# Kernel optimization log

Measured on AMD Instinct MI355X. Metric: run time of the kernel, lower is better.

The kernel has to match this reference:

```python
import jax, jax.numpy as jnp
import numpy as np

B, L, D, H = 2, 1024, 1024, 16
HD = D // H
HIDDEN = 4 * D
EPS = 1e-6
SCALE = HD ** -0.5

# RoPE tables (head_dim is even, so rope_dim == head_dim)
_inv_freq = 1.0 / (10000.0 ** (np.arange(0, HD, 2, dtype=np.float32) / HD))
_freqs = np.arange(L, dtype=np.float32)[:, None] * _inv_freq[None, :]          # [L, HD/2]
COS = jnp.asarray(np.concatenate([np.cos(_freqs), np.cos(_freqs)], -1))        # [L, HD]
SIN = jnp.asarray(np.concatenate([np.sin(_freqs), np.sin(_freqs)], -1))
MASK = jnp.tril(jnp.ones((L, L), dtype=bool))                                   # causal


def _clin(xr, xi, Wr, Wi, br=None, bi=None):
    # complex linear: (a+bi)(c+di), weights stored [out, in] as in torch
    r = xr @ Wr.T - xi @ Wi.T
    i = xr @ Wi.T + xi @ Wr.T
    if br is not None:
        r = r + br
        i = i + bi
    return r, i


def _cln(xr, xi, gr, gi, br, bi):
    mr = xr.mean(-1, keepdims=True)
    mi = xi.mean(-1, keepdims=True)
    cr = xr - mr
    ci = xi - mi
    var = (cr * cr + ci * ci).mean(-1, keepdims=True)
    s = jnp.sqrt(var + EPS)
    nr = cr / s
    ni = ci / s
    return nr * gr - ni * gi + br, nr * gi + ni * gr + bi


def _rot_half(x):
    h = x.shape[-1] // 2
    return jnp.concatenate([-x[..., h:], x[..., :h]], -1)


def _rope(xr, xi):
    # apply same real rotation to real and imag parts (matches torch code)
    return (xr * COS + _rot_half(xr) * SIN, xi * COS + _rot_half(xi) * SIN)


def _split_heads(x):
    return x.reshape(B, L, H, HD).transpose(0, 2, 1, 3)  # [B,H,L,HD]


def _merge_heads(x):
    return x.transpose(0, 2, 1, 3).reshape(B, L, D)


def setup_inputs() -> dict:
    key = jax.random.key(0)
    ks = jax.random.split(key, 20)
    n = lambda k, shape, s=1.0: jax.random.normal(k, shape, dtype=jnp.float32) * s
    s_attn = (2.0 * (D + D)) ** -0.5
    s_fc1 = (2.0 * (D + HIDDEN)) ** -0.5
    s_fc2 = (2.0 * (HIDDEN + D)) ** -0.5
    return {
        'x_real': n(ks[0], (B, L, D)),
        'x_imag': n(ks[1], (B, L, D)),
        'Wq_r': n(ks[2], (D, D), s_attn), 'Wq_i': n(ks[3], (D, D), s_attn),
        'Wk_r': n(ks[4], (D, D), s_attn), 'Wk_i': n(ks[5], (D, D), s_attn),
        'Wv_r': n(ks[6], (D, D), s_attn), 'Wv_i': n(ks[7], (D, D), s_attn),
        'Wo_r': n(ks[8], (D, D), s_attn), 'Wo_i': n(ks[9], (D, D), s_attn),
        'bo_r': jnp.zeros((D,), jnp.float32), 'bo_i': jnp.zeros((D,), jnp.float32),
        'ln1_gr': jnp.ones((D,), jnp.float32), 'ln1_gi': jnp.zeros((D,), jnp.float32),
        'ln1_br': jnp.zeros((D,), jnp.float32), 'ln1_bi': jnp.zeros((D,), jnp.float32),
        'ln2_gr': jnp.ones((D,), jnp.float32), 'ln2_gi': jnp.zeros((D,), jnp.float32),
        'ln2_br': jnp.zeros((D,), jnp.float32), 'ln2_bi': jnp.zeros((D,), jnp.float32),
        'W1_r': n(ks[10], (HIDDEN, D), s_fc1), 'W1_i': n(ks[11], (HIDDEN, D), s_fc1),
        'b1_r': jnp.zeros((HIDDEN,), jnp.float32), 'b1_i': jnp.zeros((HIDDEN,), jnp.float32),
        'W2_r': n(ks[12], (D, HIDDEN), s_fc2), 'W2_i': n(ks[13], (D, HIDDEN), s_fc2),
        'b2_r': jnp.zeros((D,), jnp.float32), 'b2_i': jnp.zeros((D,), jnp.float32),
        'mod_b': n(ks[14], (HIDDEN,), 0.1),
    }


def reference(x_real, x_imag,
              Wq_r, Wq_i, Wk_r, Wk_i, Wv_r, Wv_i, Wo_r, Wo_i, bo_r, bo_i,
              ln1_gr, ln1_gi, ln1_br, ln1_bi, ln2_gr, ln2_gi, ln2_br, ln2_bi,
              W1_r, W1_i, b1_r, b1_i, W2_r, W2_i, b2_r, b2_i, mod_b):
    # --- attention sublayer (pre-LN) ---
    hr, hi = _cln(x_real, x_imag, ln1_gr, ln1_gi, ln1_br, ln1_bi)
    Qr, Qi = _clin(hr, hi, Wq_r, Wq_i)
    Kr, Ki = _clin(hr, hi, Wk_r, Wk_i)
    Vr, Vi = _clin(hr, hi, Wv_r, Wv_i)
    Qr, Qi, Kr, Ki = map(_split_heads, (Qr, Qi, Kr, Ki))
    Vr, Vi = _split_heads(Vr), _split_heads(Vi)
    Qr, Qi = _rope(Qr, Qi)
    Kr, Ki = _rope(Kr, Ki)
    # Hermitian inner product real part: Re(Q K*) = Qr.Kr + Qi.Ki
    scores = (jnp.einsum('bhld,bhmd->bhlm', Qr, Kr)
              + jnp.einsum('bhld,bhmd->bhlm', Qi, Ki)) * SCALE
    scores = jnp.where(MASK, scores, -jnp.inf)
    attn = jax.nn.softmax(scores, axis=-1)
    out_r = _merge_heads(jnp.einsum('bhlm,bhmd->bhld', attn, Vr))
    out_i = _merge_heads(jnp.einsum('bhlm,bhmd->bhld', attn, Vi))
    out_r, out_i = _clin(out_r, out_i, Wo_r, Wo_i, bo_r, bo_i)
    ar = x_real + out_r
    ai = x_imag + out_i
    # --- feed-forward sublayer (pre-LN) ---
    hr, hi = _cln(ar, ai, ln2_gr, ln2_gi, ln2_br, ln2_bi)
    fr, fi = _clin(hr, hi, W1_r, W1_i, b1_r, b1_i)
    # ModReLU: relu(|z| + b) * e^{i angle(z)}
    mag = jnp.sqrt(fr * fr + fi * fi)
    safe = jnp.where(mag > 0, mag, 1.0)
    act = jax.nn.relu(mag + mod_b)
    fr, fi = act * fr / safe, act * fi / safe
    fr, fi = _clin(fr, fi, W2_r, W2_i, b2_r, b2_i)
    return ar + fr, ai + fi
```

## Files before the change

kernel.cpp:

```cpp
#include <hip/hip_runtime.h>

#define Bq 2
#define Lq 1024
#define Dq 1024
#define Hq 16
#define HDq 64
#define HIDq 4096
#define Mq (Bq*Lq)

typedef __bf16 bf16x8 __attribute__((ext_vector_type(8)));
typedef float floatx4 __attribute__((ext_vector_type(4)));

__device__ __forceinline__ float us2f(unsigned short u){
  unsigned v = ((unsigned)u) << 16;
  return __builtin_bit_cast(float, v);
}
__device__ __forceinline__ unsigned short f2us(float f){
  unsigned u = __builtin_bit_cast(unsigned, f);
  u = u + 0x7fffu + ((u >> 16) & 1u);
  return (unsigned short)(u >> 16);
}

__global__ __launch_bounds__(256) void cvt4_kernel(
    const float* __restrict__ s0, const float* __restrict__ s1,
    const float* __restrict__ s2, const float* __restrict__ s3,
    unsigned short* __restrict__ d0, unsigned short* __restrict__ d1,
    unsigned short* __restrict__ d2, unsigned short* __restrict__ d3,
    int n)
{
  const int a = blockIdx.y;
  const float* s = (a==0) ? s0 : (a==1) ? s1 : (a==2) ? s2 : s3;
  unsigned short* d = (a==0) ? d0 : (a==1) ? d1 : (a==2) ? d2 : d3;
  const int i = (blockIdx.x * 256 + threadIdx.x) * 8;
  if (i >= n) return;
  float4 v0 = ((const float4*)(s + i))[0];
  float4 v1 = ((const float4*)(s + i))[1];
  ushort4 o0, o1;
  o0.x=f2us(v0.x); o0.y=f2us(v0.y); o0.z=f2us(v0.z); o0.w=f2us(v0.w);
  o1.x=f2us(v1.x); o1.y=f2us(v1.y); o1.z=f2us(v1.z); o1.w=f2us(v1.w);
  ((ushort4*)(d + i))[0] = o0;
  ((ushort4*)(d + i))[1] = o1;
}

__global__ __launch_bounds__(256) void cln_kernel(
    const float* __restrict__ xr, const float* __restrict__ xi,
    const float* __restrict__ gr, const float* __restrict__ gi,
    const float* __restrict__ br, const float* __restrict__ bi,
    unsigned short* __restrict__ outr, unsigned short* __restrict__ outi)
{
  const int row = blockIdx.x;
  const int t = threadIdx.x;
  const int lane = t & 63, wv = t >> 6;
  __shared__ float sred[8];

  float4 v4r = ((const float4*)(xr + (size_t)row*Dq))[t];
  float4 v4i = ((const float4*)(xi + (size_t)row*Dq))[t];
  float vr[4] = {v4r.x, v4r.y, v4r.z, v4r.w};
  float vi[4] = {v4i.x, v4i.y, v4i.z, v4i.w};
  float sr = vr[0]+vr[1]+vr[2]+vr[3];
  float si = vi[0]+vi[1]+vi[2]+vi[3];
  #pragma unroll
  for (int o=32;o>0;o>>=1){ sr += __shfl_down(sr,o,64); si += __shfl_down(si,o,64); }
  if (lane==0){ sred[wv]=sr; sred[4+wv]=si; }
  __syncthreads();
  float mr = (sred[0]+sred[1]+sred[2]+sred[3]) * (1.0f/Dq);
  float mi = (sred[4]+sred[5]+sred[6]+sred[7]) * (1.0f/Dq);
  float cr[4], ci[4], vs = 0.f;
  #pragma unroll
  for (int j=0;j<4;++j){ cr[j]=vr[j]-mr; ci[j]=vi[j]-mi; vs += cr[j]*cr[j]+ci[j]*ci[j]; }
  #pragma unroll
  for (int o=32;o>0;o>>=1) vs += __shfl_down(vs,o,64);
  __syncthreads();
  if (lane==0) sred[wv]=vs;
  __syncthreads();
  float var = (sred[0]+sred[1]+sred[2]+sred[3]) * (1.0f/Dq);
  float inv = rsqrtf(var + 1e-6f);

  float4 g4r = ((const float4*)gr)[t];
  float4 g4i = ((const float4*)gi)[t];
  float4 b4r = ((const float4*)br)[t];
  float4 b4i = ((const float4*)bi)[t];
  float grf[4] = {g4r.x,g4r.y,g4r.z,g4r.w};
  float gif[4] = {g4i.x,g4i.y,g4i.z,g4i.w};
  float brf[4] = {b4r.x,b4r.y,b4r.z,b4r.w};
  float bif[4] = {b4i.x,b4i.y,b4i.z,b4i.w};
  ushort4 o_r, o_i;
  unsigned short orr[4], oii[4];
  #pragma unroll
  for (int j=0;j<4;++j){
    float nr = cr[j]*inv, ni = ci[j]*inv;
    orr[j] = f2us(nr*grf[j] - ni*gif[j] + brf[j]);
    oii[j] = f2us(nr*gif[j] + ni*grf[j] + bif[j]);
  }
  o_r.x=orr[0]; o_r.y=orr[1]; o_r.z=orr[2]; o_r.w=orr[3];
  o_i.x=oii[0]; o_i.y=oii[1]; o_i.z=oii[2]; o_i.w=oii[3];
  ((ushort4*)(outr + (size_t)row*Dq))[t] = o_r;
  ((ushort4*)(outi + (size_t)row*Dq))[t] = o_i;
}

template<int EPI, bool ROPE>
__global__ __launch_bounds__(256,2) void cgemm_kernel(
    const unsigned short* __restrict__ Ar, const unsigned short* __restrict__ Ai,
    const unsigned short* __restrict__ Wr, const unsigned short* __restrict__ Wi,
    void* __restrict__ Cr, void* __restrict__ Ci,
    const float* __restrict__ biasR, const float* __restrict__ biasI,
    const float* __restrict__ resR, const float* __restrict__ resI,
    const float* __restrict__ modb,
    int Ndim, int Kdim)
{
  const int t = threadIdx.x;
  const int wv = t >> 6, lane = t & 63;
  const int quad = lane >> 4, l15 = lane & 15;
  const int m0 = blockIdx.x * 64, n0 = blockIdx.y * 64;

  __shared__ __align__(16) unsigned short sAr[64*40], sAi[64*40], sWr[64*40], sWi[64*40];

  floatx4 accRR[4], accII[4], accRI[4], accIR[4];
  floatx4 zero = {0.f,0.f,0.f,0.f};
  #pragma unroll
  for (int i=0;i<4;++i){ accRR[i]=zero; accII[i]=zero; accRI[i]=zero; accIR[i]=zero; }

  const int lr = t >> 2;
  const int lc = (t & 3) * 8;
  const unsigned short* pAr = Ar + (size_t)(m0+lr)*Kdim + lc;
  const unsigned short* pAi = Ai + (size_t)(m0+lr)*Kdim + lc;
  const unsigned short* pWr = Wr + (size_t)(n0+lr)*Kdim + lc;
  const unsigned short* pWi = Wi + (size_t)(n0+lr)*Kdim + lc;
  const int ldso = lr*40 + lc;
  const int arow = wv*16 + l15;

  const int nk = Kdim >> 5;
  for (int kk=0; kk<nk; ++kk){
    uint4 va = *(const uint4*)(pAr + kk*32);
    uint4 vb = *(const uint4*)(pAi + kk*32);
    uint4 vc = *(const uint4*)(pWr + kk*32);
    uint4 vd = *(const uint4*)(pWi + kk*32);
    __syncthreads();
    *(uint4*)&sAr[ldso] = va;
    *(uint4*)&sAi[ldso] = vb;
    *(uint4*)&sWr[ldso] = vc;
    *(uint4*)&sWi[ldso] = vd;
    __syncthreads();
    bf16x8 fAr = *(const bf16x8*)&sAr[arow*40 + quad*8];
    bf16x8 fAi = *(const bf16x8*)&sAi[arow*40 + quad*8];
    #pragma unroll
    for (int tt=0; tt<4; ++tt){
      const int brow = tt*16 + l15;
      bf16x8 fWr = *(const bf16x8*)&sWr[brow*40 + quad*8];
      bf16x8 fWi = *(const bf16x8*)&sWi[brow*40 + quad*8];
      accRR[tt] = __builtin_amdgcn_mfma_f32_16x16x32_bf16(fAr, fWr, accRR[tt], 0,0,0);
      accII[tt] = __builtin_amdgcn_mfma_f32_16x16x32_bf16(fAi, fWi, accII[tt], 0,0,0);
      accRI[tt] = __builtin_amdgcn_mfma_f32_16x16x32_bf16(fAr, fWi, accRI[tt], 0,0,0);
      accIR[tt] = __builtin_amdgcn_mfma_f32_16x16x32_bf16(fAi, fWr, accIR[tt], 0,0,0);
    }
  }

  float cr[4][4], ci[4][4];
  #pragma unroll
  for (int tt=0; tt<4; ++tt)
    #pragma unroll
    for (int r=0; r<4; ++r){
      cr[tt][r] = accRR[tt][r] - accII[tt][r];
      ci[tt][r] = accRI[tt][r] + accIR[tt][r];
    }

  if (ROPE){
    #pragma unroll
    for (int tt=0; tt<2; ++tt){
      const int j = tt*16 + l15;
      const float invf = powf(10000.0f, -(float)j * (1.0f/32.0f));
      #pragma unroll
      for (int r=0; r<4; ++r){
        const int gm = m0 + wv*16 + quad*4 + r;
        const int l = gm & (Lq-1);
        float s, c;
        sincosf((float)l * invf, &s, &c);
        float xr_ = cr[tt][r], yr_ = cr[tt+2][r];
        cr[tt][r]   = xr_*c - yr_*s;
        cr[tt+2][r] = yr_*c + xr_*s;
        float xi_ = ci[tt][r], yi_ = ci[tt+2][r];
        ci[tt][r]   = xi_*c - yi_*s;
        ci[tt+2][r] = yi_*c + xi_*s;
      }
    }
  }

  #pragma unroll
  for (int tt=0; tt<4; ++tt){
    const int gn = n0 + tt*16 + l15;
    float bR = 0.f, bI = 0.f, mb = 0.f;
    if (EPI >= 1){ bR = biasR[gn]; bI = biasI[gn]; }
    if (EPI == 2){ mb = modb[gn]; }
    #pragma unroll
    for (int r=0; r<4; ++r){
      const int gm = m0 + wv*16 + quad*4 + r;
      const size_t idx = (size_t)gm*Ndim + gn;
      float vr_ = cr[tt][r] + bR, vi_ = ci[tt][r] + bI;
      if (EPI == 1 || EPI == 3){ vr_ += resR[idx]; vi_ += resI[idx]; }
      if (EPI == 2){
        float mag = sqrtf(vr_*vr_ + vi_*vi_);
        float safe = (mag > 0.f) ? mag : 1.0f;
        float act = fmaxf(mag + mb, 0.f);
        float sc = act / safe;
        vr_ *= sc; vi_ *= sc;
      }
      if (EPI == 0 || EPI == 2){
        ((unsigned short*)Cr)[idx] = f2us(vr_);
        ((unsigned short*)Ci)[idx] = f2us(vi_);
      } else {
        ((float*)Cr)[idx] = vr_;
        ((float*)Ci)[idx] = vi_;
      }
    }
  }
}

__global__ __launch_bounds__(256) void vtrans_kernel(
    const unsigned short* __restrict__ Vr, const unsigned short* __restrict__ Vi,
    unsigned short* __restrict__ VTr, unsigned short* __restrict__ VTi)
{
  const int lt = blockIdx.x;
  const int bh = blockIdx.y;
  const int h = bh & (Hq-1), b = bh >> 4;
  const int t = threadIdx.x;
  __shared__ unsigned short sTr[64*65], sTi[64*65];

  const int row = t >> 2;
  const int dc  = (t & 3) * 16;
  const size_t g = ((size_t)(b*Lq) + lt*64 + row)*Dq + h*HDq + dc;
  uint4 a0 = *(const uint4*)(Vr + g);
  uint4 a1 = *(const uint4*)(Vr + g + 8);
  uint4 b0 = *(const uint4*)(Vi + g);
  uint4 b1 = *(const uint4*)(Vi + g + 8);
  const unsigned short* pa0 = (const unsigned short*)&a0;
  const unsigned short* pa1 = (const unsigned short*)&a1;
  const unsigned short* pb0 = (const unsigned short*)&b0;
  const unsigned short* pb1 = (const unsigned short*)&b1;
  #pragma unroll
  for (int e=0;e<8;++e){
    sTr[(dc+e)*65 + row]   = pa0[e];
    sTr[(dc+8+e)*65 + row] = pa1[e];
    sTi[(dc+e)*65 + row]   = pb0[e];
    sTi[(dc+8+e)*65 + row] = pb1[e];
  }
  __syncthreads();
  const int d  = t >> 2;
  const int lc = (t & 3) * 16;
  unsigned short bufr[16], bufi[16];
  #pragma unroll
  for (int e=0;e<16;++e){
    bufr[e] = sTr[d*65 + lc + e];
    bufi[e] = sTi[d*65 + lc + e];
  }
  const size_t og = ((size_t)bh*HDq + d)*Lq + lt*64 + lc;
  *(uint4*)(VTr + og)     = *(const uint4*)&bufr[0];
  *(uint4*)(VTr + og + 8) = *(const uint4*)&bufr[8];
  *(uint4*)(VTi + og)     = *(const uint4*)&bufi[0];
  *(uint4*)(VTi + og + 8) = *(const uint4*)&bufi[8];
}

__device__ __forceinline__ int swz(int v){ return v ^ ((v >> 4) & 7); }

__global__ __launch_bounds__(256,2) void fattn_kernel(
    const unsigned short* __restrict__ Qr, const unsigned short* __restrict__ Qi,
    const unsigned short* __restrict__ Kr, const unsigned short* __restrict__ Ki,
    const unsigned short* __restrict__ VTr, const unsigned short* __restrict__ VTi,
    unsigned short* __restrict__ Or, unsigned short* __restrict__ Oi)
{
  const int qt = (int)(gridDim.x - 1 - blockIdx.x);
  const int bh = blockIdx.y;
  const int h = bh & (Hq-1), b = bh >> 4;
  const int t = threadIdx.x;
  const int w = t >> 6, lane = t & 63;
  const int quad = lane >> 4, l15 = lane & 15;

  __shared__ __align__(16) unsigned short sKr[4096], sKi[4096], sVr[4096], sVi[4096];
  __shared__ __align__(16) unsigned short sP[64*72];

  const size_t qbase = ((size_t)(b*Lq) + qt*64 + w*16 + l15)*Dq + h*HDq;
  bf16x8 qr_lo = *(const bf16x8*)(Qr + qbase + quad*8);
  bf16x8 qr_hi = *(const bf16x8*)(Qr + qbase + 32 + quad*8);
  bf16x8 qi_lo = *(const bf16x8*)(Qi + qbase + quad*8);
  bf16x8 qi_hi = *(const bf16x8*)(Qi + qbase + 32 + quad*8);

  const floatx4 fzero = {0.f,0.f,0.f,0.f};
  floatx4 aOr[4], aOi[4];
  #pragma unroll
  for (int i=0;i<4;++i){ aOr[i]=fzero; aOi[i]=fzero; }
  float m_run[4] = {-1e30f,-1e30f,-1e30f,-1e30f};
  float l_run[4] = {0.f,0.f,0.f,0.f};

  const int srow = t >> 2;
  const int sns  = srow >> 4;
  const int sl15 = srow & 15;
  const int q8   = (t & 3) * 2;
  const int dstA = sns*1024 + swz(q8*16 + sl15)*8;
  const int dstB = sns*1024 + swz((q8+1)*16 + sl15)*8;

  const int rd0 = swz(quad*16 + l15)*8;
  const int rd1 = swz((4+quad)*16 + l15)*8;

  for (int kt = 0; kt <= qt; ++kt){
    const size_t kg = ((size_t)(b*Lq) + kt*64 + srow)*Dq + h*HDq + q8*8;
    uint4 ka = *(const uint4*)(Kr + kg);
    uint4 kb = *(const uint4*)(Kr + kg + 8);
    uint4 kc = *(const uint4*)(Ki + kg);
    uint4 kd = *(const uint4*)(Ki + kg + 8);
    const size_t vg = ((size_t)bh*HDq + srow)*Lq + kt*64 + q8*8;
    uint4 va = *(const uint4*)(VTr + vg);
    uint4 vb = *(const uint4*)(VTr + vg + 8);
    uint4 vc = *(const uint4*)(VTi + vg);
    uint4 vd = *(const uint4*)(VTi + vg + 8);
    __syncthreads();
    *(uint4*)&sKr[dstA] = ka;  *(uint4*)&sKr[dstB] = kb;
    *(uint4*)&sKi[dstA] = kc;  *(uint4*)&sKi[dstB] = kd;
    *(uint4*)&sVr[dstA] = va;  *(uint4*)&sVr[dstB] = vb;
    *(uint4*)&sVi[dstA] = vc;  *(uint4*)&sVi[dstB] = vd;
    __syncthreads();

    floatx4 sc[4];
    #pragma unroll
    for (int ns=0; ns<4; ++ns){
      floatx4 x = fzero;
      x = __builtin_amdgcn_mfma_f32_16x16x32_bf16(qr_lo, *(const bf16x8*)&sKr[ns*1024 + rd0], x, 0,0,0);
      x = __builtin_amdgcn_mfma_f32_16x16x32_bf16(qr_hi, *(const bf16x8*)&sKr[ns*1024 + rd1], x, 0,0,0);
      x = __builtin_amdgcn_mfma_f32_16x16x32_bf16(qi_lo, *(const bf16x8*)&sKi[ns*1024 + rd0], x, 0,0,0);
      x = __builtin_amdgcn_mfma_f32_16x16x32_bf16(qi_hi, *(const bf16x8*)&sKi[ns*1024 + rd1], x, 0,0,0);
      sc[ns] = x;
    }

    const bool diag = (kt == qt);
    float rmax[4] = {-1e30f,-1e30f,-1e30f,-1e30f};
    #pragma unroll
    for (int ns=0; ns<4; ++ns){
      #pragma unroll
      for (int r=0; r<4; ++r){
        float s = sc[ns][r] * 0.125f;
        if (diag && (ns*16 + l15 > w*16 + quad*4 + r)) s = -1e30f;
        sc[ns][r] = s;
        rmax[r] = fmaxf(rmax[r], s);
      }
    }
    #pragma unroll
    for (int off=1; off<16; off<<=1){
      #pragma unroll
      for (int r=0; r<4; ++r) rmax[r] = fmaxf(rmax[r], __shfl_xor(rmax[r], off, 64));
    }

    float alpha[4], rsum[4];
    #pragma unroll
    for (int r=0; r<4; ++r){
      float mn = fmaxf(m_run[r], rmax[r]);
      alpha[r] = __expf(m_run[r] - mn);
      m_run[r] = mn;
      rsum[r] = 0.f;
    }
    #pragma unroll
    for (int ns=0; ns<4; ++ns){
      #pragma unroll
      for (int r=0; r<4; ++r){
        float p = __expf(sc[ns][r] - m_run[r]);
        rsum[r] += p;
        sP[(w*16 + quad*4 + r)*72 + ns*16 + l15] = f2us(p);
      }
    }
    #pragma unroll
    for (int off=1; off<16; off<<=1){
      #pragma unroll
      for (int r=0; r<4; ++r) rsum[r] += __shfl_xor(rsum[r], off, 64);
    }
    #pragma unroll
    for (int r=0; r<4; ++r) l_run[r] = l_run[r]*alpha[r] + rsum[r];
    #pragma unroll
    for (int ds=0; ds<4; ++ds)
      #pragma unroll
      for (int r=0; r<4; ++r){ aOr[ds][r] *= alpha[r]; aOi[ds][r] *= alpha[r]; }

    #pragma unroll
    for (int step=0; step<2; ++step){
      bf16x8 pf = *(const bf16x8*)&sP[(w*16 + l15)*72 + step*32 + quad*8];
      const int ro = (step==0) ? rd0 : rd1;
      #pragma unroll
      for (int ds=0; ds<4; ++ds){
        aOr[ds] = __builtin_amdgcn_mfma_f32_16x16x32_bf16(pf, *(const bf16x8*)&sVr[ds*1024 + ro], aOr[ds], 0,0,0);
        aOi[ds] = __builtin_amdgcn_mfma_f32_16x16x32_bf16(pf, *(const bf16x8*)&sVi[ds*1024 + ro], aOi[ds], 0,0,0);
      }
    }
  }

  #pragma unroll
  for (int r=0; r<4; ++r){
    const float il = 1.0f / l_run[r];
    const size_t ob = ((size_t)(b*Lq) + qt*64 + w*16 + quad*4 + r)*Dq + h*HDq;
    #pragma unroll
    for (int ds=0; ds<4; ++ds){
      Or[ob + ds*16 + l15] = f2us(aOr[ds][r] * il);
      Oi[ob + ds*16 + l15] = f2us(aOi[ds][r] * il);
    }
  }
}

extern "C" void kernel_launch(void* const* d_in, const int* in_sizes, int n_in,
                              void* d_out, int out_size, void* d_ws, size_t ws_size,
                              hipStream_t stream)
{
  const float* x_r    = (const float*)d_in[0];
  const float* x_i    = (const float*)d_in[1];
  const float* Wq_r   = (const float*)d_in[2];
  const float* Wq_i   = (const float*)d_in[3];
  const float* Wk_r   = (const float*)d_in[4];
  const float* Wk_i   = (const float*)d_in[5];
  const float* Wv_r   = (const float*)d_in[6];
  const float* Wv_i   = (const float*)d_in[7];
  const float* Wo_r   = (const float*)d_in[8];
  const float* Wo_i   = (const float*)d_in[9];
  const float* bo_r   = (const float*)d_in[10];
  const float* bo_i   = (const float*)d_in[11];
  const float* ln1_gr = (const float*)d_in[12];
  const float* ln1_gi = (const float*)d_in[13];
  const float* ln1_br = (const float*)d_in[14];
  const float* ln1_bi = (const float*)d_in[15];
  const float* ln2_gr = (const float*)d_in[16];
  const float* ln2_gi = (const float*)d_in[17];
  const float* ln2_br = (const float*)d_in[18];
  const float* ln2_bi = (const float*)d_in[19];
  const float* W1_r   = (const float*)d_in[20];
  const float* W1_i   = (const float*)d_in[21];
  const float* b1_r   = (const float*)d_in[22];
  const float* b1_i   = (const float*)d_in[23];
  const float* W2_r   = (const float*)d_in[24];
  const float* W2_i   = (const float*)d_in[25];
  const float* b2_r   = (const float*)d_in[26];
  const float* b2_i   = (const float*)d_in[27];
  const float* mod_b  = (const float*)d_in[28];

  char* wsb = (char*)d_ws;
  const size_t MB = 1024*1024;
  unsigned short* bWq_r = (unsigned short*)(wsb + 0*MB);
  unsigned short* bWq_i = (unsigned short*)(wsb + 2*MB);
  unsigned short* bWk_r = (unsigned short*)(wsb + 4*MB);
  unsigned short* bWk_i = (unsigned short*)(wsb + 6*MB);
  unsigned short* bWv_r = (unsigned short*)(wsb + 8*MB);
  unsigned short* bWv_i = (unsigned short*)(wsb + 10*MB);
  unsigned short* bWo_r = (unsigned short*)(wsb + 12*MB);
  unsigned short* bWo_i = (unsigned short*)(wsb + 14*MB);
  unsigned short* bW1_r = (unsigned short*)(wsb + 16*MB);
  unsigned short* bW1_i = (unsigned short*)(wsb + 24*MB);
  unsigned short* bW2_r = (unsigned short*)(wsb + 32*MB);
  unsigned short* bW2_i = (unsigned short*)(wsb + 40*MB);
  unsigned short* hr  = (unsigned short*)(wsb + 48*MB);
  unsigned short* hi_ = (unsigned short*)(wsb + 52*MB);
  unsigned short* Qr  = (unsigned short*)(wsb + 56*MB);
  unsigned short* Qi  = (unsigned short*)(wsb + 60*MB);
  unsigned short* Kr  = (unsigned short*)(wsb + 64*MB);
  unsigned short* Ki  = (unsigned short*)(wsb + 68*MB);
  unsigned short* Vr  = (unsigned short*)(wsb + 72*MB);
  unsigned short* Vi  = (unsigned short*)(wsb + 76*MB);
  unsigned short* VTr = (unsigned short*)(wsb + 80*MB);
  unsigned short* VTi = (unsigned short*)(wsb + 84*MB);
  unsigned short* Or  = hr;
  unsigned short* Oi  = hi_;
  unsigned short* h2r = Qr;
  unsigned short* h2i = Qi;
  unsigned short* fr  = (unsigned short*)(wsb + 64*MB);
  unsigned short* fi  = (unsigned short*)(wsb + 80*MB);

  float* outR = (float*)d_out;
  float* outI = outR + (size_t)Mq*Dq;

  const dim3 blk(256);
  const dim3 gD(Mq/64, Dq/64);
  const dim3 gH(Mq/64, HIDq/64);

  const int nDD = Dq*Dq;
  const int nDH = Dq*HIDq;
  cvt4_kernel<<<dim3(nDD/2048, 4), blk, 0, stream>>>(Wq_r, Wq_i, Wk_r, Wk_i,
      bWq_r, bWq_i, bWk_r, bWk_i, nDD);
  cvt4_kernel<<<dim3(nDD/2048, 4), blk, 0, stream>>>(Wv_r, Wv_i, Wo_r, Wo_i,
      bWv_r, bWv_i, bWo_r, bWo_i, nDD);
  cvt4_kernel<<<dim3(nDH/2048, 4), blk, 0, stream>>>(W1_r, W1_i, W2_r, W2_i,
      bW1_r, bW1_i, bW2_r, bW2_i, nDH);

  cln_kernel<<<Mq, blk, 0, stream>>>(x_r, x_i, ln1_gr, ln1_gi, ln1_br, ln1_bi, hr, hi_);
  cgemm_kernel<0,true ><<<gD, blk, 0, stream>>>(hr, hi_, bWq_r, bWq_i, Qr, Qi,
      nullptr, nullptr, nullptr, nullptr, nullptr, Dq, Dq);
  cgemm_kernel<0,true ><<<gD, blk, 0, stream>>>(hr, hi_, bWk_r, bWk_i, Kr, Ki,
      nullptr, nullptr, nullptr, nullptr, nullptr, Dq, Dq);
  cgemm_kernel<0,false><<<gD, blk, 0, stream>>>(hr, hi_, bWv_r, bWv_i, Vr, Vi,
      nullptr, nullptr, nullptr, nullptr, nullptr, Dq, Dq);
  vtrans_kernel<<<dim3(16, 32), blk, 0, stream>>>(Vr, Vi, VTr, VTi);
  fattn_kernel<<<dim3(16, 32), blk, 0, stream>>>(Qr, Qi, Kr, Ki, VTr, VTi, Or, Oi);
  cgemm_kernel<1,false><<<gD, blk, 0, stream>>>(Or, Oi, bWo_r, bWo_i, outR, outI,
      bo_r, bo_i, x_r, x_i, nullptr, Dq, Dq);
  cln_kernel<<<Mq, blk, 0, stream>>>(outR, outI, ln2_gr, ln2_gi, ln2_br, ln2_bi, h2r, h2i);
  cgemm_kernel<2,false><<<gH, blk, 0, stream>>>(h2r, h2i, bW1_r, bW1_i, fr, fi,
      b1_r, b1_i, nullptr, nullptr, mod_b, HIDq, Dq);
  cgemm_kernel<3,false><<<gD, blk, 0, stream>>>(fr, fi, bW2_r, bW2_i, outR, outI,
      b2_r, b2_i, outR, outI, nullptr, Dq, HIDq);
}
```

Baseline: 552.4 us.

## Recast FFN complex GEMMs as real GEMMs over concatenated real/imag weights

The feed-forward complex linears are re-expressed as single real GEMMs. Activations are stored as interleaved [real | imag] rows (K=2048), and the weights are pre-packed into block matrices [[Wr,-Wi],[Wi,Wr]] with interleaved output columns. A new rgemm kernel stages tiles with direct global-to-LDS loads and larger 128-wide N tiles. It applies ModReLU by pairing the adjacent real and imaginary outputs through a lane shuffle. This removes the four-accumulator complex GEMM structure and its redundant A/W tile loads, at the cost of a larger packed weight buffer built on every call and an unpipelined single-buffered K loop.

```diff
diff --git a/kernel.cpp b/kernel.cpp
--- a/kernel.cpp
+++ b/kernel.cpp
@@ -19,6 +19,12 @@
   unsigned u = __builtin_bit_cast(unsigned, f);
   u = u + 0x7fffu + ((u >> 16) & 1u);
   return (unsigned short)(u >> 16);
+}
+
+__device__ __forceinline__ void glds16(const unsigned short* g, unsigned short* l){
+  __builtin_amdgcn_global_load_lds(
+      (const __attribute__((address_space(1))) unsigned int*)g,
+      (__attribute__((address_space(3))) unsigned int*)l, 16, 0, 0);
 }
 
 __global__ __launch_bounds__(256) void cvt4_kernel(
@@ -42,11 +48,64 @@
   ((ushort4*)(d + i))[1] = o1;
 }
 
+__global__ __launch_bounds__(256) void w1cat_kernel(
+    const float* __restrict__ Wr, const float* __restrict__ Wi,
+    unsigned short* __restrict__ dst)
+{
+  const int tid = blockIdx.x*256 + threadIdx.x;
+  const int u = tid >> 7;
+  const int k = (tid & 127) * 8;
+  float4 r0 = *(const float4*)(Wr + (size_t)u*1024 + k);
+  float4 r1 = *(const float4*)(Wr + (size_t)u*1024 + k + 4);
+  float4 i0 = *(const float4*)(Wi + (size_t)u*1024 + k);
+  float4 i1 = *(const float4*)(Wi + (size_t)u*1024 + k + 4);
+  ushort4 R0 = {f2us(r0.x),f2us(r0.y),f2us(r0.z),f2us(r0.w)};
+  ushort4 R1 = {f2us(r1.x),f2us(r1.y),f2us(r1.z),f2us(r1.w)};
+  ushort4 I0 = {f2us(i0.x),f2us(i0.y),f2us(i0.z),f2us(i0.w)};
+  ushort4 I1 = {f2us(i1.x),f2us(i1.y),f2us(i1.z),f2us(i1.w)};
+  ushort4 N0 = {f2us(-i0.x),f2us(-i0.y),f2us(-i0.z),f2us(-i0.w)};
+  ushort4 N1 = {f2us(-i1.x),f2us(-i1.y),f2us(-i1.z),f2us(-i1.w)};
+  unsigned short* p0 = dst + (size_t)(2*u)*2048;
+  unsigned short* p1 = dst + (size_t)(2*u+1)*2048;
+  *(ushort4*)(p0 + k) = R0;          *(ushort4*)(p0 + k + 4) = R1;
+  *(ushort4*)(p0 + 1024 + k) = N0;   *(ushort4*)(p0 + 1024 + k + 4) = N1;
+  *(ushort4*)(p1 + k) = I0;          *(ushort4*)(p1 + k + 4) = I1;
+  *(ushort4*)(p1 + 1024 + k) = R0;   *(ushort4*)(p1 + 1024 + k + 4) = R1;
+}
+
+__global__ __launch_bounds__(256) void w2cat_kernel(
+    const float* __restrict__ Wr, const float* __restrict__ Wi,
+    unsigned short* __restrict__ dst)
+{
+  const int tid = blockIdx.x*256 + threadIdx.x;
+  const int n = tid >> 9;
+  const int u = (tid & 511) * 8;
+  float4 r0 = *(const float4*)(Wr + (size_t)n*4096 + u);
+  float4 r1 = *(const float4*)(Wr + (size_t)n*4096 + u + 4);
+  float4 i0 = *(const float4*)(Wi + (size_t)n*4096 + u);
+  float4 i1 = *(const float4*)(Wi + (size_t)n*4096 + u + 4);
+  unsigned short a[16], b[16];
+  const float rr[8] = {r0.x,r0.y,r0.z,r0.w,r1.x,r1.y,r1.z,r1.w};
+  const float ii[8] = {i0.x,i0.y,i0.z,i0.w,i1.x,i1.y,i1.z,i1.w};
+  #pragma unroll
+  for (int e=0;e<8;++e){
+    a[2*e]   = f2us(rr[e]);  a[2*e+1] = f2us(-ii[e]);
+    b[2*e]   = f2us(ii[e]);  b[2*e+1] = f2us(rr[e]);
+  }
+  unsigned short* p0 = dst + (size_t)n*8192 + 2*u;
+  unsigned short* p1 = dst + (size_t)(1024+n)*8192 + 2*u;
+  *(uint4*)(p0)     = *(const uint4*)&a[0];
+  *(uint4*)(p0 + 8) = *(const uint4*)&a[8];
+  *(uint4*)(p1)     = *(const uint4*)&b[0];
+  *(uint4*)(p1 + 8) = *(const uint4*)&b[8];
+}
+
 __global__ __launch_bounds__(256) void cln_kernel(
     const float* __restrict__ xr, const float* __restrict__ xi,
     const float* __restrict__ gr, const float* __restrict__ gi,
     const float* __restrict__ br, const float* __restrict__ bi,
-    unsigned short* __restrict__ outr, unsigned short* __restrict__ outi)
+    unsigned short* __restrict__ outr, unsigned short* __restrict__ outi,
+    int ostride)
 {
   const int row = blockIdx.x;
   const int t = threadIdx.x;
@@ -94,8 +153,8 @@
   }
   o_r.x=orr[0]; o_r.y=orr[1]; o_r.z=orr[2]; o_r.w=orr[3];
   o_i.x=oii[0]; o_i.y=oii[1]; o_i.z=oii[2]; o_i.w=oii[3];
-  ((ushort4*)(outr + (size_t)row*Dq))[t] = o_r;
-  ((ushort4*)(outi + (size_t)row*Dq))[t] = o_i;
+  ((ushort4*)(outr + (size_t)row*ostride))[t] = o_r;
+  ((ushort4*)(outi + (size_t)row*ostride))[t] = o_i;
 }
 
 template<int EPI, bool ROPE>
@@ -105,7 +164,6 @@
     void* __restrict__ Cr, void* __restrict__ Ci,
     const float* __restrict__ biasR, const float* __restrict__ biasI,
     const float* __restrict__ resR, const float* __restrict__ resI,
-    const float* __restrict__ modb,
     int Ndim, int Kdim)
 {
   const int t = threadIdx.x;
@@ -188,28 +246,111 @@
   #pragma unroll
   for (int tt=0; tt<4; ++tt){
     const int gn = n0 + tt*16 + l15;
-    float bR = 0.f, bI = 0.f, mb = 0.f;
+    float bR = 0.f, bI = 0.f;
     if (EPI >= 1){ bR = biasR[gn]; bI = biasI[gn]; }
-    if (EPI == 2){ mb = modb[gn]; }
     #pragma unroll
     for (int r=0; r<4; ++r){
       const int gm = m0 + wv*16 + quad*4 + r;
       const size_t idx = (size_t)gm*Ndim + gn;
       float vr_ = cr[tt][r] + bR, vi_ = ci[tt][r] + bI;
-      if (EPI == 1 || EPI == 3){ vr_ += resR[idx]; vi_ += resI[idx]; }
-      if (EPI == 2){
-        float mag = sqrtf(vr_*vr_ + vi_*vi_);
-        float safe = (mag > 0.f) ? mag : 1.0f;
-        float act = fmaxf(mag + mb, 0.f);
-        float sc = act / safe;
-        vr_ *= sc; vi_ *= sc;
-      }
-      if (EPI == 0 || EPI == 2){
+      if (EPI == 1){ vr_ += resR[idx]; vi_ += resI[idx]; }
+      if (EPI == 0){
         ((unsigned short*)Cr)[idx] = f2us(vr_);
         ((unsigned short*)Ci)[idx] = f2us(vi_);
       } else {
         ((float*)Cr)[idx] = vr_;
         ((float*)Ci)[idx] = vi_;
+      }
+    }
+  }
+}
+
+template<int EPI, int BMt>
+__global__ __launch_bounds__(256,2) void rgemm_kernel(
+    const unsigned short* __restrict__ A,
+    const unsigned short* __restrict__ W,
+    void* __restrict__ C0, void* __restrict__ C1,
+    const float* __restrict__ bias0, const float* __restrict__ bias1,
+    const float* __restrict__ res0, const float* __restrict__ res1,
+    const float* __restrict__ modb,
+    int Ndim, int Kdim)
+{
+  constexpr int TA = BMt/32;
+  constexpr int GA = BMt/16;
+  constexpr int NC = (GA + 8) / 4;
+  const int t = threadIdx.x;
+  const int w = t >> 6, lane = t & 63;
+  const int wr = w >> 1, wc = w & 1;
+  const int quad = lane >> 4, l15 = lane & 15;
+  const int m0 = blockIdx.x * BMt, n0 = blockIdx.y * 128;
+
+  __shared__ __align__(16) unsigned short sA[BMt*32];
+  __shared__ __align__(16) unsigned short sW[128*32];
+
+  floatx4 acc[TA][4];
+  const floatx4 fzero = {0.f,0.f,0.f,0.f};
+  #pragma unroll
+  for (int ta=0; ta<TA; ++ta)
+    #pragma unroll
+    for (int tb=0; tb<4; ++tb) acc[ta][tb] = fzero;
+
+  const int sl = lane & 15, sc8 = (lane >> 4) * 8;
+
+  for (int kk = 0; kk < (Kdim >> 5); ++kk){
+    const int k0 = kk*32;
+    __syncthreads();
+    #pragma unroll
+    for (int c = 0; c < NC; ++c){
+      const int cg = c*4 + w;
+      if (cg < GA)
+        glds16(A + (size_t)(m0 + cg*16 + sl)*Kdim + k0 + sc8, &sA[cg*512]);
+      else
+        glds16(W + (size_t)(n0 + (cg-GA)*16 + sl)*Kdim + k0 + sc8, &sW[(cg-GA)*512]);
+    }
+    __syncthreads();
+    bf16x8 af[TA], wf[4];
+    #pragma unroll
+    for (int ta=0; ta<TA; ++ta) af[ta] = *(const bf16x8*)&sA[(wr*TA + ta)*512 + lane*8];
+    #pragma unroll
+    for (int tb=0; tb<4; ++tb)  wf[tb] = *(const bf16x8*)&sW[(wc*4 + tb)*512 + lane*8];
+    #pragma unroll
+    for (int ta=0; ta<TA; ++ta)
+      #pragma unroll
+      for (int tb=0; tb<4; ++tb)
+        acc[ta][tb] = __builtin_amdgcn_mfma_f32_16x16x32_bf16(af[ta], wf[tb], acc[ta][tb], 0,0,0);
+  }
+
+  const int Nh = Ndim >> 1;
+  #pragma unroll
+  for (int ta=0; ta<TA; ++ta){
+    #pragma unroll
+    for (int tb=0; tb<4; ++tb){
+      const int gn = n0 + wc*64 + tb*16 + l15;
+      if (EPI == 1){
+        const bool hi = gn >= Nh;
+        const int col = hi ? gn - Nh : gn;
+        const float bs = hi ? bias1[col] : bias0[col];
+        const float* rp = hi ? res1 : res0;
+        float* op = hi ? (float*)C1 : (float*)C0;
+        #pragma unroll
+        for (int r=0; r<4; ++r){
+          const int gm = m0 + wr*(BMt/2) + ta*16 + quad*4 + r;
+          op[(size_t)gm*Nh + col] = acc[ta][tb][r] + bs + rp[(size_t)gm*Nh + col];
+        }
+      } else {
+        const int u = gn >> 1;
+        const float bs = (gn & 1) ? bias1[u] : bias0[u];
+        const float mb = modb[u];
+        #pragma unroll
+        for (int r=0; r<4; ++r){
+          const int gm = m0 + wr*(BMt/2) + ta*16 + quad*4 + r;
+          float v = acc[ta][tb][r] + bs;
+          float p = __shfl_xor(v, 1, 64);
+          float mag = sqrtf(v*v + p*p);
+          float act = fmaxf(mag + mb, 0.f);
+          float sc = act / (mag > 0.f ? mag : 1.f);
+          ((unsigned short*)C0)[(size_t)gm*Ndim + gn] = f2us(v*sc);
+        }
       }
     }
   }
@@ -444,57 +585,52 @@
   unsigned short* bWv_i = (unsigned short*)(wsb + 10*MB);
   unsigned short* bWo_r = (unsigned short*)(wsb + 12*MB);
   unsigned short* bWo_i = (unsigned short*)(wsb + 14*MB);
-  unsigned short* bW1_r = (unsigned short*)(wsb + 16*MB);
-  unsigned short* bW1_i = (unsigned short*)(wsb + 24*MB);
-  unsigned short* bW2_r = (unsigned short*)(wsb + 32*MB);
-  unsigned short* bW2_i = (unsigned short*)(wsb + 40*MB);
-  unsigned short* hr  = (unsigned short*)(wsb + 48*MB);
-  unsigned short* hi_ = (unsigned short*)(wsb + 52*MB);
-  unsigned short* Qr  = (unsigned short*)(wsb + 56*MB);
-  unsigned short* Qi  = (unsigned short*)(wsb + 60*MB);
-  unsigned short* Kr  = (unsigned short*)(wsb + 64*MB);
-  unsigned short* Ki  = (unsigned short*)(wsb + 68*MB);
-  unsigned short* Vr  = (unsigned short*)(wsb + 72*MB);
-  unsigned short* Vi  = (unsigned short*)(wsb + 76*MB);
-  unsigned short* VTr = (unsigned short*)(wsb + 80*MB);
-  unsigned short* VTi = (unsigned short*)(wsb + 84*MB);
+  unsigned short* W1cat = (unsigned short*)(wsb + 16*MB);
+  unsigned short* W2cat = (unsigned short*)(wsb + 48*MB);
+  unsigned short* hr  = (unsigned short*)(wsb + 80*MB);
+  unsigned short* hi_ = (unsigned short*)(wsb + 84*MB);
+  unsigned short* Qr  = (unsigned short*)(wsb + 88*MB);
+  unsigned short* Qi  = (unsigned short*)(wsb + 92*MB);
+  unsigned short* Kr  = (unsigned short*)(wsb + 96*MB);
+  unsigned short* Ki  = (unsigned short*)(wsb + 100*MB);
+  unsigned short* Vr  = (unsigned short*)(wsb + 104*MB);
+  unsigned short* Vi  = (unsigned short*)(wsb + 108*MB);
+  unsigned short* VTr = (unsigned short*)(wsb + 112*MB);
+  unsigned short* VTi = (unsigned short*)(wsb + 116*MB);
   unsigned short* Or  = hr;
   unsigned short* Oi  = hi_;
-  unsigned short* h2r = Qr;
-  unsigned short* h2i = Qi;
-  unsigned short* fr  = (unsigned short*)(wsb + 64*MB);
-  unsigned short* fi  = (unsigned short*)(wsb + 80*MB);
+  unsigned short* h2  = (unsigned short*)(wsb + 80*MB);
+  unsigned short* f   = (unsigned short*)(wsb + 88*MB);
 
   float* outR = (float*)d_out;
   float* outI = outR + (size_t)Mq*Dq;
 
   const dim3 blk(256);
   const dim3 gD(Mq/64, Dq/64);
-  const dim3 gH(Mq/64, HIDq/64);
 
   const int nDD = Dq*Dq;
-  const int nDH = Dq*HIDq;
   cvt4_kernel<<<dim3(nDD/2048, 4), blk, 0, stream>>>(Wq_r, Wq_i, Wk_r, Wk_i,
       bWq_r, bWq_i, bWk_r, bWk_i, nDD);
   cvt4_kernel<<<dim3(nDD/2048, 4), blk, 0, stream>>>(Wv_r, Wv_i, Wo_r, Wo_i,
       bWv_r, bWv_i, bWo_r, bWo_i, nDD);
-  cvt4_kernel<<<dim3(nDH/2048, 4), blk, 0, stream>>>(W1_r, W1_i, W2_r, W2_i,
-      bW1_r, bW1_i, bW2_r, bW2_i, nDH);
-
-  cln_kernel<<<Mq, blk, 0, stream>>>(x_r, x_i, ln1_gr, ln1_gi, ln1_br, ln1_bi, hr, hi_);
+  w1cat_kernel<<<2048, blk, 0, stream>>>(W1_r, W1_i, W1cat);
+  w2cat_kernel<<<2048, blk, 0, stream>>>(W2_r, W2_i, W2cat);
+
+  cln_kernel<<<Mq, blk, 0, stream>>>(x_r, x_i, ln1_gr, ln1_gi, ln1_br, ln1_bi, hr, hi_, 1024);
   cgemm_kernel<0,true ><<<gD, blk, 0, stream>>>(hr, hi_, bWq_r, bWq_i, Qr, Qi,
-      nullptr, nullptr, nullptr, nullptr, nullptr, Dq, Dq);
+      nullptr, nullptr, nullptr, nullptr, Dq, Dq);
   cgemm_kernel<0,true ><<<gD, blk, 0, stream>>>(hr, hi_, bWk_r, bWk_i, Kr, Ki,
-      nullptr, nullptr, nullptr, nullptr, nullptr, Dq, Dq);
+      nullptr, nullptr, nullptr, nullptr, Dq, Dq);
   cgemm_kernel<0,false><<<gD, blk, 0, stream>>>(hr, hi_, bWv_r, bWv_i, Vr, Vi,
-      nullptr, nullptr, nullptr, nullptr, nullptr, Dq, Dq);
+      nullptr, nullptr, nullptr, nullptr, Dq, Dq);
   vtrans_kernel<<<dim3(16, 32), blk, 0, stream>>>(Vr, Vi, VTr, VTi);
   fattn_kernel<<<dim3(16, 32), blk, 0, stream>>>(Qr, Qi, Kr, Ki, VTr, VTi, Or, Oi);
   cgemm_kernel<1,false><<<gD, blk, 0, stream>>>(Or, Oi, bWo_r, bWo_i, outR, outI,
-      bo_r, bo_i, x_r, x_i, nullptr, Dq, Dq);
-  cln_kernel<<<Mq, blk, 0, stream>>>(outR, outI, ln2_gr, ln2_gi, ln2_br, ln2_bi, h2r, h2i);
-  cgemm_kernel<2,false><<<gH, blk, 0, stream>>>(h2r, h2i, bW1_r, bW1_i, fr, fi,
-      b1_r, b1_i, nullptr, nullptr, mod_b, HIDq, Dq);
-  cgemm_kernel<3,false><<<gD, blk, 0, stream>>>(fr, fi, bW2_r, bW2_i, outR, outI,
-      b2_r, b2_i, outR, outI, nullptr, Dq, HIDq);
-}
+      bo_r, bo_i, x_r, x_i, Dq, Dq);
+  cln_kernel<<<Mq, blk, 0, stream>>>(outR, outI, ln2_gr, ln2_gi, ln2_br, ln2_bi,
+      h2, h2 + 1024, 2048);
+  rgemm_kernel<2,128><<<dim3(Mq/128, 8192/128), blk, 0, stream>>>(
+      h2, W1cat, f, nullptr, b1_r, b1_i, nullptr, nullptr, mod_b, 8192, 2048);
+  rgemm_kernel<1,64><<<dim3(Mq/64, 2048/128), blk, 0, stream>>>(
+      f, W2cat, outR, outI, b2_r, b2_i, outR, outI, nullptr, 2048, 8192);
+}
```

New measurement: 699.5 us. +26.6%, slower.
